# Kernel optimization log

Measured on AMD Instinct MI355X. Metric: run time of the kernel, lower is better.

Reference implementation:

```python
import jax, jax.numpy as jnp
import numpy as np

INP = 256
OUP = 256
FGROUP = 16
CGROUP = 8
K = 3
STRIDE = 1
PAD = K // 2
B, H, W = 16, 64, 64
O1 = OUP * INP * K * K // CGROUP  # 73728, glgf output channels


def setup_inputs() -> dict:
    key = jax.random.key(0)
    ks = jax.random.split(key, 11)
    s = 0.1  # keep sigmoid pre-activations in a sane range
    return {
        "x": jax.random.normal(ks[0], (B, INP, H, W), jnp.float32),
        # GLGF generating the dynamic conv weights (oup*inp*k*k//cgroup outputs)
        "g1_fc1_l": jax.random.normal(ks[1], (INP, INP // FGROUP), jnp.float32) * s,
        "g1_fc1_g1": jax.random.normal(ks[2], (FGROUP, INP // FGROUP), jnp.float32) * s,
        "g1_fc1_g2": jax.random.normal(ks[3], (INP, FGROUP), jnp.float32) * s,
        "g1_fc2_l": jax.random.normal(ks[4], (O1,), jnp.float32) * s,
        "g1_fc2_g": jax.random.normal(ks[5], (INP,), jnp.float32) * s,
        # GLGF generating the per-channel output gate c (oup outputs)
        "g2_fc1_l": jax.random.normal(ks[6], (INP, INP // FGROUP), jnp.float32) * s,
        "g2_fc1_g1": jax.random.normal(ks[7], (FGROUP, INP // FGROUP), jnp.float32) * s,
        "g2_fc1_g2": jax.random.normal(ks[8], (INP, FGROUP), jnp.float32) * s,
        "g2_fc2_l": jax.random.normal(ks[9], (OUP,), jnp.float32) * s,
        "g2_fc2_g": jax.random.normal(ks[10], (INP,), jnp.float32) * s,
    }


def glgf(g, w1l, w1g1, w1g2, w2l, w2g):
    """GLGF applied to a [B, inp] gap vector (all convs are 1x1 -> grouped linears)."""
    b, inp = g.shape
    gp = inp // FGROUP
    gg = g.reshape(b, FGROUP, gp)
    # wn_fc1_l: grouped (fgroup) inp->inp; weight [inp, inp//fgroup]
    local = jnp.einsum('bgi,goi->bgo', gg, w1l.reshape(FGROUP, gp, gp)).reshape(b, inp)
    # wn_fc1_g2(wn_fc1_g1(x)): inp->fgroup (grouped) then fgroup->inp (dense)
    glob = jnp.einsum('bgi,gi->bg', gg, w1g1) @ w1g2.T  # [b, inp]
    h = jax.nn.sigmoid(local + glob)
    # wn_fc2_l: groups=inp, inp->O; weight [O] (1 input channel per output)
    O = w2l.shape[0]
    local2 = (h[:, :, None] * w2l.reshape(inp, O // inp)).reshape(b, O)
    # wn_fc2_g: dense inp->1, broadcast-added
    glob2 = h @ w2g  # [b]
    return local2 + glob2[:, None]


def reference(x, g1_fc1_l, g1_fc1_g1, g1_fc1_g2, g1_fc2_l, g1_fc2_g,
              g2_fc1_l, g2_fc1_g1, g2_fc1_g2, g2_fc2_l, g2_fc2_g):
    b = x.shape[0]
    gap = x.mean(axis=(2, 3))  # adaptive_avg_pool2d to 1x1 -> [b, inp]
    # generate per-sample grouped conv weights: [b, oup, inp//cgroup, k, k]
    xw = glgf(gap, g1_fc1_l, g1_fc1_g1, g1_fc1_g2, g1_fc2_l, g1_fc2_g)
    w = xw.reshape(b, OUP, INP // CGROUP, K, K)
    # torch's groups=b*cgroup batch-trick == per-sample conv with groups=cgroup
    def conv_one(xi, wi):
        return jax.lax.conv_general_dilated(
            xi[None], wi, (STRIDE, STRIDE), [(PAD, PAD), (PAD, PAD)],
            feature_group_count=CGROUP,
            dimension_numbers=('NCHW', 'OIHW', 'NCHW'))[0]
    y = jax.vmap(conv_one)(x, w)  # [b, oup, H, W]
    # per-sample, per-channel gate
    c = glgf(gap, g2_fc1_l, g2_fc1_g1, g2_fc1_g2, g2_fc2_l, g2_fc2_g)  # [b, oup]
    return y * c[:, :, None, None]
```

## Files before the change

### kernel.cpp

```cpp
#include <hip/hip_runtime.h>
#include <cstddef>
#include <cstdint>

typedef __attribute__((ext_vector_type(8))) short bf16x8;
typedef __attribute__((ext_vector_type(4))) unsigned short ushort4v;
typedef __attribute__((ext_vector_type(8))) unsigned short ushort8v;
typedef __attribute__((ext_vector_type(16))) float f32x16;

__device__ __forceinline__ unsigned short f2bf(float f) {
  union { float f; unsigned u; } v; v.f = f;
  unsigned r = v.u + 0x7FFFu + ((v.u >> 16) & 1u);
  return (unsigned short)(r >> 16);
}

__device__ __forceinline__ void gload16(const void* g, void* l) {
  __builtin_amdgcn_global_load_lds(
      (const __attribute__((address_space(1))) void*)(unsigned long long)(uintptr_t)g,
      (__attribute__((address_space(3))) void*)(unsigned)(uintptr_t)l, 16, 0, 0);
}

#define PADC 132
__global__ __launch_bounds__(256) void prep_kernel(
    const float* __restrict__ x, unsigned short* __restrict__ xt,
    float* __restrict__ partials) {
  __shared__ unsigned short cm[32 * PADC];
  __shared__ float sred[32][32];
  const int bid = blockIdx.x;
  const int wkr = ((bid & 7) << 9) | (bid >> 3);
  const int yp = wkr & 31, g = (wkr >> 5) & 7, b = wkr >> 8;
  const int y0 = yp * 2;
  const int tid = threadIdx.x;
  const float* xg = x + (size_t)(b * 256 + g * 32) * 4096;

  float csum[4];
#pragma unroll
  for (int j = 0; j < 4; ++j) {
    const int idx = tid + 256 * j;
    const int ic = idx >> 5;
    const int r = idx & 31;
    const int ry = r >> 4, gx4 = (r & 15) * 4;
    const float4 v = *reinterpret_cast<const float4*>(
        xg + (size_t)ic * 4096 + (y0 + ry) * 64 + gx4);
    csum[j] = v.x + v.y + v.z + v.w;
    ushort4v s;
    s[0] = f2bf(v.x); s[1] = f2bf(v.y); s[2] = f2bf(v.z); s[3] = f2bf(v.w);
    *reinterpret_cast<ushort4v*>(&cm[ic * PADC + ry * 64 + gx4]) = s;
  }
#pragma unroll
  for (int j = 0; j < 4; ++j) {
    const int ic = (tid >> 5) + 8 * j;
    sred[ic][tid & 31] = csum[j];
  }
  __syncthreads();

  if (tid < 32) {
    float s = 0.f;
#pragma unroll
    for (int i = 0; i < 32; ++i) s += sred[tid][i];
    partials[(size_t)(b * 256 + g * 32 + tid) * 32 + yp] = s;
  }

  const size_t xtb = (size_t)(b * 8 + g) * (66 * 66 * 32);
#pragma unroll
  for (int jj = 0; jj < 2; ++jj) {
    const int o = tid + 256 * jj;
    const int px = o >> 2, icq = o & 3;
    const int ry = px >> 6, gx = px & 63;
    ushort8v t;
#pragma unroll
    for (int c2 = 0; c2 < 8; ++c2) t[c2] = cm[(icq * 8 + c2) * PADC + px];
    *reinterpret_cast<ushort8v*>(
        &xt[xtb + ((size_t)(y0 + ry + 1) * 66 + (gx + 1)) * 32 + icq * 8]) = t;
  }

  const ushort8v z = {0, 0, 0, 0, 0, 0, 0, 0};
  if (tid < 16) {
    const int rr = tid >> 3;
    const int side = (tid >> 2) & 1;
    const int icq = tid & 3;
    const int col = side * 65;
    *reinterpret_cast<ushort8v*>(
        &xt[xtb + ((size_t)(y0 + rr + 1) * 66 + col) * 32 + icq * 8]) = z;
  }
  if (yp == 0 || yp == 31) {
    const int row = (yp == 0) ? 0 : 65;
    for (int o = tid; o < 66 * 4; o += 256) {
      const int col = o >> 2, icq = o & 3;
      *reinterpret_cast<ushort8v*>(
          &xt[xtb + ((size_t)row * 66 + col) * 32 + icq * 8]) = z;
    }
  }
}

__global__ __launch_bounds__(256) void glgf_pack(
    const float* __restrict__ partials,
    const float* __restrict__ w1l, const float* __restrict__ w1g1,
    const float* __restrict__ w1g2, const float* __restrict__ w2l,
    const float* __restrict__ w2g,
    const float* __restrict__ v1l, const float* __restrict__ v1g1,
    const float* __restrict__ v1g2, const float* __restrict__ v2l,
    const float* __restrict__ v2g,
    unsigned short* __restrict__ wpack) {
  __shared__ float gapL[256];
  __shared__ float t1L[16];
  __shared__ float h1L[256];
  __shared__ float red[256];
  __shared__ float cLs[32];
  const int bid = blockIdx.x;
  const int bg = ((bid & 7) << 4) | (bid >> 3);
  const int g = bg & 7, b = bg >> 3;
  const int c = threadIdx.x;
  {
    float s = 0.f;
    const float* pp = partials + (size_t)(b * 256 + c) * 32;
#pragma unroll
    for (int i = 0; i < 32; ++i) s += pp[i];
    gapL[c] = s * (1.f / 4096.f);
  }
  __syncthreads();

  const int gbase = c & ~15;
  float local1 = 0.f;
#pragma unroll
  for (int i = 0; i < 16; ++i) local1 += gapL[gbase + i] * w1l[c * 16 + i];
  if (c < 16) {
    float t = 0.f;
#pragma unroll
    for (int i = 0; i < 16; ++i) t += gapL[c * 16 + i] * w1g1[c * 16 + i];
    t1L[c] = t;
  }
  __syncthreads();
  float glob1 = 0.f;
#pragma unroll
  for (int gg = 0; gg < 16; ++gg) glob1 += t1L[gg] * w1g2[c * 16 + gg];
  const float h1 = 1.f / (1.f + expf(-(local1 + glob1)));
  h1L[c] = h1;
  red[c] = h1 * w2g[c];
  __syncthreads();
  for (int s = 128; s > 0; s >>= 1) {
    if (c < s) red[c] += red[c + s];
    __syncthreads();
  }
  const float glob2 = red[0];

  float local2 = 0.f;
#pragma unroll
  for (int i = 0; i < 16; ++i) local2 += gapL[gbase + i] * v1l[c * 16 + i];
  if (c < 16) {
    float t = 0.f;
#pragma unroll
    for (int i = 0; i < 16; ++i) t += gapL[c * 16 + i] * v1g1[c * 16 + i];
    t1L[c] = t;
  }
  __syncthreads();
  float glob1b = 0.f;
#pragma unroll
  for (int gg = 0; gg < 16; ++gg) glob1b += t1L[gg] * v1g2[c * 16 + gg];
  const float h2 = 1.f / (1.f + expf(-(local2 + glob1b)));
  red[c] = h2 * v2g[c];
  __syncthreads();
  for (int s = 128; s > 0; s >>= 1) {
    if (c < s) red[c] += red[c + s];
    __syncthreads();
  }
  if (c < 32) {
    const int o = g * 32 + c;
    float l = 0.f;
#pragma unroll
    for (int i = 0; i < 16; ++i) l += gapL[(o & ~15) + i] * v1l[o * 16 + i];
    float gl = 0.f;
#pragma unroll
    for (int gg = 0; gg < 16; ++gg) gl += t1L[gg] * v1g2[o * 16 + gg];
    const float h2o = 1.f / (1.f + expf(-(l + gl)));
    cLs[c] = h2o * v2l[o] + red[0];
  }
  __syncthreads();

  unsigned short* wpo = wpack + (size_t)bg * 9216;
#pragma unroll 4
  for (int it = 0; it < 36; ++it) {
    const int idx = it * 256 + c;
    const int kk = idx >> 9;
    const int rem = idx & 511;
    const int l = rem >> 3, e = rem & 7;
    const int oc = l & 31, hi = l >> 5;
    const int ic = ((kk & 1) << 4) + hi * 8 + e;
    const int sp = kk >> 1;
    const int o = (g << 5) + oc;
    const float wv = h1L[o] * w2l[o * 288 + ic * 9 + sp] + glob2;
    wpo[idx] = f2bf(wv * cLs[oc]);
  }
}

__global__ __launch_bounds__(256, 8) void conv_kernel(
    const unsigned short* __restrict__ wpack,
    const unsigned short* __restrict__ xt, float* __restrict__ out) {
  __shared__ __align__(16) unsigned short btile[8448];

  const int bid = blockIdx.x;
  const int wkr = ((bid & 7) << 9) | (bid >> 3);
  const int yp = wkr & 31;
  const int bg = wkr >> 5;
  const int g = bg & 7, b = bg >> 3;
  const int tid = threadIdx.x;
  const int lane = tid & 63, wave = tid >> 6;
  const int n = lane & 31, hi = lane >> 5;
  const int wr = wave >> 1, wc = wave & 1;

  const char* xbase = (const char*)xt + (size_t)bg * 278784;
  const int ys = yp * 2;

#pragma unroll
  for (int i = 0; i < 5; ++i) {
    const int li = i * 256 + tid;
    if (li < 1056) {
      const int r = li / 264, rem = li - r * 264;
      const int cqs = rem / 66, px = rem % 66;
      const int cq = cqs ^ (px & 3);
      gload16(xbase + (ys + r) * 4224 + px * 64 + cq * 16,
              (char*)btile + i * 4096 + wave * 1024);
    }
  }
  asm volatile("s_waitcnt vmcnt(0) lgkmcnt(0)\n\ts_barrier" ::: "memory");
  __builtin_amdgcn_sched_barrier(0);

  const unsigned short* wp = wpack + (size_t)bg * 9216 + lane * 8;
  f32x16 acc;
#pragma unroll
  for (int i = 0; i < 16; ++i) acc[i] = 0.f;

#pragma unroll
  for (int kk = 0; kk < 18; ++kk) {
    const int sp = kk >> 1;
    const int ky = sp / 3, kx = sp % 3;
    const int px2 = wc * 32 + n + kx;
    const int cq = ((kk & 1) << 1) + hi;
    const bf16x8 af = *reinterpret_cast<const bf16x8*>(wp + kk * 512);
    const bf16x8 bf = *reinterpret_cast<const bf16x8*>(
        &btile[((((wr + ky) << 2) + (cq ^ (px2 & 3))) * 66 + px2) * 8]);
    acc = __builtin_amdgcn_mfma_f32_32x32x16_bf16(af, bf, acc, 0, 0, 0);
  }

  const int y = ys + wr;
  float* ob = out + (size_t)(b * 256 + g * 32) * 4096 + y * 64 + wc * 32 + n +
              (size_t)(hi << 2) * 4096;
#pragma unroll
  for (int r = 0; r < 16; ++r) {
    const int row = (r & 3) + ((r >> 2) << 3);
    ob[(size_t)row * 4096] = acc[r];
  }
}

extern "C" void kernel_launch(void* const* d_in, const int* in_sizes, int n_in,
                              void* d_out, int out_size, void* d_ws,
                              size_t ws_size, hipStream_t stream) {
  const float* x    = (const float*)d_in[0];
  const float* w1l  = (const float*)d_in[1];
  const float* w1g1 = (const float*)d_in[2];
  const float* w1g2 = (const float*)d_in[3];
  const float* w2l  = (const float*)d_in[4];
  const float* w2g  = (const float*)d_in[5];
  const float* v1l  = (const float*)d_in[6];
  const float* v1g1 = (const float*)d_in[7];
  const float* v1g2 = (const float*)d_in[8];
  const float* v2l  = (const float*)d_in[9];
  const float* v2g  = (const float*)d_in[10];
  float* out = (float*)d_out;

  unsigned short* xt = (unsigned short*)d_ws;
  float* partials = (float*)(xt + 17842176);
  unsigned short* wpack = (unsigned short*)(partials + 131072);

  prep_kernel<<<4096, 256, 0, stream>>>(x, xt, partials);
  glgf_pack<<<128, 256, 0, stream>>>(partials, w1l, w1g1, w1g2, w2l, w2g,
                                     v1l, v1g1, v1g2, v2l, v2g, wpack);
  conv_kernel<<<4096, 256, 0, stream>>>(wpack, xt, out);
}
```

Baseline: 55.83 us.

## Enlarge conv tile to four rows per block with weights preloaded in registers

Each conv block now covers four output rows instead of two, with each wave computing a full 64-pixel row via two accumulators. The grid is halved and the halo reuse improves: six input rows are staged for four output rows instead of four for two. All 18 weight fragments are loaded into registers before the LDS tile load, so weight fetches overlap the input staging, and each A fragment is reused for two MFMAs. The MFMA loop runs at raised wave priority. Register pressure and LDS per block grow, and launch bounds drop to 3 blocks per SIMD, which reduces occupancy and latency hiding.

```diff
diff --git a/kernel.cpp b/kernel.cpp
--- a/kernel.cpp
+++ b/kernel.cpp
@@ -192,62 +192,74 @@
   }
 }
 
-__global__ __launch_bounds__(256, 8) void conv_kernel(
+__global__ __launch_bounds__(256, 3) void conv_kernel(
     const unsigned short* __restrict__ wpack,
     const unsigned short* __restrict__ xt, float* __restrict__ out) {
-  __shared__ __align__(16) unsigned short btile[8448];
+  __shared__ __align__(16) unsigned short btile[12672];
 
   const int bid = blockIdx.x;
-  const int wkr = ((bid & 7) << 9) | (bid >> 3);
-  const int yp = wkr & 31;
-  const int bg = wkr >> 5;
+  const int wkr = ((bid & 7) << 8) | (bid >> 3);
+  const int yb = wkr & 15;
+  const int bg = wkr >> 4;
   const int g = bg & 7, b = bg >> 3;
   const int tid = threadIdx.x;
   const int lane = tid & 63, wave = tid >> 6;
   const int n = lane & 31, hi = lane >> 5;
-  const int wr = wave >> 1, wc = wave & 1;
 
   const char* xbase = (const char*)xt + (size_t)bg * 278784;
-  const int ys = yp * 2;
-
-#pragma unroll
-  for (int i = 0; i < 5; ++i) {
+  const int y0 = yb * 4;
+
+  const unsigned short* wp = wpack + (size_t)bg * 9216 + lane * 8;
+  bf16x8 a[18];
+#pragma unroll
+  for (int kk = 0; kk < 18; ++kk) {
+    a[kk] = *reinterpret_cast<const bf16x8*>(wp + kk * 512);
+    asm volatile("" : "+v"(a[kk]));
+  }
+
+#pragma unroll
+  for (int i = 0; i < 7; ++i) {
     const int li = i * 256 + tid;
-    if (li < 1056) {
+    if (li < 1584) {
       const int r = li / 264, rem = li - r * 264;
       const int cqs = rem / 66, px = rem % 66;
       const int cq = cqs ^ (px & 3);
-      gload16(xbase + (ys + r) * 4224 + px * 64 + cq * 16,
+      gload16(xbase + (y0 + r) * 4224 + px * 64 + cq * 16,
               (char*)btile + i * 4096 + wave * 1024);
     }
   }
   asm volatile("s_waitcnt vmcnt(0) lgkmcnt(0)\n\ts_barrier" ::: "memory");
   __builtin_amdgcn_sched_barrier(0);
 
-  const unsigned short* wp = wpack + (size_t)bg * 9216 + lane * 8;
-  f32x16 acc;
-#pragma unroll
-  for (int i = 0; i < 16; ++i) acc[i] = 0.f;
-
+  f32x16 acc0, acc1;
+#pragma unroll
+  for (int i = 0; i < 16; ++i) { acc0[i] = 0.f; acc1[i] = 0.f; }
+
+  __builtin_amdgcn_s_setprio(1);
 #pragma unroll
   for (int kk = 0; kk < 18; ++kk) {
     const int sp = kk >> 1;
     const int ky = sp / 3, kx = sp % 3;
-    const int px2 = wc * 32 + n + kx;
     const int cq = ((kk & 1) << 1) + hi;
-    const bf16x8 af = *reinterpret_cast<const bf16x8*>(wp + kk * 512);
-    const bf16x8 bf = *reinterpret_cast<const bf16x8*>(
-        &btile[((((wr + ky) << 2) + (cq ^ (px2 & 3))) * 66 + px2) * 8]);
-    acc = __builtin_amdgcn_mfma_f32_32x32x16_bf16(af, bf, acc, 0, 0, 0);
-  }
-
-  const int y = ys + wr;
-  float* ob = out + (size_t)(b * 256 + g * 32) * 4096 + y * 64 + wc * 32 + n +
+    const int pxA = n + kx;
+    const int pxB = 32 + n + kx;
+    const bf16x8 bf0 = *reinterpret_cast<const bf16x8*>(
+        &btile[((((wave + ky) << 2) + (cq ^ (pxA & 3))) * 66 + pxA) * 8]);
+    const bf16x8 bf1 = *reinterpret_cast<const bf16x8*>(
+        &btile[((((wave + ky) << 2) + (cq ^ (pxB & 3))) * 66 + pxB) * 8]);
+    acc0 = __builtin_amdgcn_mfma_f32_32x32x16_bf16(a[kk], bf0, acc0, 0, 0, 0);
+    acc1 = __builtin_amdgcn_mfma_f32_32x32x16_bf16(a[kk], bf1, acc1, 0, 0, 0);
+  }
+  __builtin_amdgcn_s_setprio(0);
+
+  const int y = y0 + wave;
+  float* ob = out + (size_t)(b * 256 + g * 32) * 4096 + y * 64 + n +
               (size_t)(hi << 2) * 4096;
 #pragma unroll
   for (int r = 0; r < 16; ++r) {
     const int row = (r & 3) + ((r >> 2) << 3);
-    ob[(size_t)row * 4096] = acc[r];
+    ob[(size_t)row * 4096] = acc0[r];
+    ob[(size_t)row * 4096 + 32] = acc1[r];
   }
 }
 
@@ -274,5 +286,5 @@
   prep_kernel<<<4096, 256, 0, stream>>>(x, xt, partials);
   glgf_pack<<<128, 256, 0, stream>>>(partials, w1l, w1g1, w1g2, w2l, w2g,
                                      v1l, v1g1, v1g2, v2l, v2g, wpack);
-  conv_kernel<<<4096, 256, 0, stream>>>(wpack, xt, out);
-}
+  conv_kernel<<<2048, 256, 0, stream>>>(wpack, xt, out);
+}
```

Result: slower. 57.51 us (+3.0%).
